# Kernel tuning notes

Hardware: AMD Instinct MI355X
Metric: run time of the kernel (lower is better)

Reference implementation:

```python
import jax, jax.numpy as jnp
import numpy as np

T, B, D, H, E = 16, 4096, 256, 512, 32
EPS = 0.1

def setup_inputs() -> dict:
    key = jax.random.key(0)
    ks = jax.random.split(key, 8)
    return {
        "term_emb": jax.random.normal(ks[0], (T, B, D), dtype=jnp.float32),
        "pred_emb": jax.random.normal(ks[1], (E, B, D), dtype=jnp.float32),
        "inv_pred_emb": jax.random.normal(ks[2], (E, B, D), dtype=jnp.float32),
        "signs": jnp.ones((E,), dtype=jnp.float32),
        "W1": jax.random.normal(ks[3], (D, H), dtype=jnp.float32) * (1.0 / np.sqrt(D)),
        "b1": jnp.zeros((H,), dtype=jnp.float32),
        "W2": jax.random.normal(ks[4], (H, D), dtype=jnp.float32) * (1.0 / np.sqrt(H)),
        "b2": jnp.zeros((D,), dtype=jnp.float32),
        "heads": jax.random.randint(ks[5], (E,), 0, T, dtype=jnp.int64),
        "tails": jax.random.randint(ks[6], (E,), 0, T, dtype=jnp.int64),
    }

def reference(term_emb, pred_emb, inv_pred_emb, signs, W1, b1, W2, b2, heads, tails):
    # gather endpoint embeddings per edge: [E, B, D]
    h = term_emb[heads]
    t = term_emb[tails]
    s = signs[:, None, None]
    # estimate_tail_emb (TransE-style NBP): translate by relation embedding
    msg_to_tail = s * (h + pred_emb)      # message along edge direction
    msg_to_head = s * (t + inv_pred_emb)  # message along inverse direction
    # scatter-add messages into per-term slots (sum aggregation)
    agg = (jax.ops.segment_sum(msg_to_tail, tails, num_segments=T)
           + jax.ops.segment_sum(msg_to_head, heads, num_segments=T))
    agg = agg + EPS * term_emb  # residual with eps
    # 1-layer MLP: Linear -> ReLU -> Linear
    hidden = jax.nn.relu(jnp.einsum('tbd,dh->tbh', agg, W1) + b1)
    out = jnp.einsum('tbh,hd->tbd', hidden, W2) + b2
    return out
```

## Files before the change

### kernel.cpp

```cpp
#include <hip/hip_runtime.h>
#include <hip/hip_bf16.h>
#include <stdint.h>

#define T_DIM 16
#define B_DIM 4096
#define D_DIM 256
#define H_DIM 512
#define E_DIM 32
#define M_DIM (T_DIM * B_DIM)
#define BD_DIM (B_DIM * D_DIM)
#define EPS_F 0.1f

#define NSLICE 16
#define SH 32
#define HS_LD 40
#define MAXS 64

typedef __attribute__((ext_vector_type(8))) short short8;
typedef __attribute__((ext_vector_type(4))) float f32x4;

#define GLOBAL_AS __attribute__((address_space(1)))
#define LDS_AS __attribute__((address_space(3)))

__device__ __forceinline__ uint32_t f2bf_rne(float x) {
  uint32_t u = __float_as_uint(x);
  return (u + 0x7fffu + ((u >> 16) & 1u)) >> 16;
}

__global__ __launch_bounds__(256) void agg_prep_kernel(
    const float* __restrict__ term, const float* __restrict__ pred,
    const float* __restrict__ inv, const float* __restrict__ signs,
    const int* __restrict__ heads, const int* __restrict__ tails,
    const float* __restrict__ W1, const float* __restrict__ W2,
    uint16_t* __restrict__ agg, uint16_t* __restrict__ W1T, uint16_t* __restrict__ W2T) {
  const int tid = threadIdx.x;
  if (blockIdx.x >= 1024) {
    const int idx = (blockIdx.x - 1024) * 256 + tid;
    const int d = idx >> 9, h = idx & (H_DIM - 1);
    W1T[h * D_DIM + d] = (uint16_t)f2bf_rne(W1[idx]);
    const int h2 = idx >> 8, d2 = idx & (D_DIM - 1);
    W2T[d2 * H_DIM + h2] = (uint16_t)f2bf_rne(W2[idx]);
    return;
  }

  __shared__ float Cm[T_DIM][T_DIM];
  __shared__ float Lsgn[T_DIM][MAXS];
  __shared__ uint64_t Lptr[T_DIM][MAXS];
  __shared__ int Lcnt[T_DIM];

  Cm[tid >> 4][tid & 15] = ((tid >> 4) == (tid & 15)) ? EPS_F : 0.f;
  if (tid < T_DIM) Lcnt[tid] = 0;
  __syncthreads();
  if (tid < E_DIM) {
    const int e = tid;
    const int hh = heads[e] & (T_DIM - 1);
    const int tt = tails[e] & (T_DIM - 1);
    const float s = signs[e];
    atomicAdd(&Cm[tt][hh], s);
    int i = atomicAdd(&Lcnt[tt], 1);
    Lsgn[tt][i] = s; Lptr[tt][i] = (uint64_t)(pred + (size_t)e * BD_DIM);
    atomicAdd(&Cm[hh][tt], s);
    i = atomicAdd(&Lcnt[hh], 1);
    Lsgn[hh][i] = s; Lptr[hh][i] = (uint64_t)(inv + (size_t)e * BD_DIM);
  }
  __syncthreads();

  const int j = (blockIdx.x * 256 + tid) * 4;

  f32x4 tr[T_DIM];
#pragma unroll
  for (int s = 0; s < T_DIM; ++s)
    tr[s] = __builtin_nontemporal_load(reinterpret_cast<const f32x4*>(term + (size_t)s * BD_DIM + j));

#pragma unroll 2
  for (int t = 0; t < T_DIM; ++t) {
    f32x4 cv[4];
#pragma unroll
    for (int q = 0; q < 4; ++q) cv[q] = *reinterpret_cast<const f32x4*>(&Cm[t][q * 4]);

    float acc[4] = {0.f, 0.f, 0.f, 0.f};
#pragma unroll
    for (int s = 0; s < T_DIM; ++s) {
      const float cs = cv[s >> 2][s & 3];
#pragma unroll
      for (int k = 0; k < 4; ++k) acc[k] += cs * tr[s][k];
    }

    const int n = Lcnt[t];
#pragma unroll 2
    for (int i = 0; i < n; ++i) {
      const float sg = Lsgn[t][i];
      const float* bp = (const float*)Lptr[t][i];
      const f32x4 p = __builtin_nontemporal_load(reinterpret_cast<const f32x4*>(bp + j));
#pragma unroll
      for (int k = 0; k < 4; ++k) acc[k] += sg * p[k];
    }

    uint2 pk;
    pk.x = f2bf_rne(acc[0]) | (f2bf_rne(acc[1]) << 16);
    pk.y = f2bf_rne(acc[2]) | (f2bf_rne(acc[3]) << 16);
    *reinterpret_cast<uint2*>(agg + (size_t)t * BD_DIM + j) = pk;
  }
}

__global__ __launch_bounds__(256, 2) void mlp_fused(
    const uint16_t* __restrict__ A,
    const uint16_t* __restrict__ W1T,
    const uint16_t* __restrict__ W2T,
    const float* __restrict__ b1, const float* __restrict__ b2,
    float* __restrict__ Out) {
  __shared__ __align__(16) uint16_t As[64 * 256];
  __shared__ __align__(16) uint16_t Hs[2][64 * HS_LD];

  const int tid = threadIdx.x;
  const int w = tid >> 6;
  const int l = tid & 63;
  const int lane16 = l & 15;
  const int quad = l >> 4;
  const int m0 = blockIdx.x * 64;

  const int wm  = (w & 1) * 32;
  const int wnA = ((w >> 1) & 1) * 16;
  const int wn2 = ((w >> 1) & 1) * 128;

#pragma unroll
  for (int p = 0; p < 8; ++p) {
    const int off = p * 2048 + tid * 8;
    const int kc = off >> 11;
    const int row = (off >> 5) & 63;
    const int c = off & 31;
    const uint16_t* g = A + (size_t)(m0 + row) * D_DIM + kc * 32 + c;
    __builtin_amdgcn_global_load_lds((const GLOBAL_AS uint32_t*)g,
                                     (LDS_AS uint32_t*)(As + off), 16, 0, 0);
  }

  short8 w1f[8];
#pragma unroll
  for (int kk = 0; kk < 8; ++kk)
    w1f[kk] = *reinterpret_cast<const short8*>(
        W1T + (size_t)(wnA + lane16) * D_DIM + kk * 32 + quad * 8);

  __syncthreads();

  f32x4 oacc[2][8];
#pragma unroll
  for (int i = 0; i < 2; ++i)
#pragma unroll
    for (int j = 0; j < 8; ++j) oacc[i][j] = (f32x4){0.f, 0.f, 0.f, 0.f};

  for (int s = 0; s < NSLICE; ++s) {
    short8 w2f[8];
#pragma unroll
    for (int j = 0; j < 8; ++j)
      w2f[j] = *reinterpret_cast<const short8*>(
          W2T + (size_t)(wn2 + j * 16 + lane16) * H_DIM + s * SH + quad * 8);

    f32x4 hacc[2];
#pragma unroll
    for (int i = 0; i < 2; ++i) hacc[i] = (f32x4){0.f, 0.f, 0.f, 0.f};
#pragma unroll
    for (int kk = 0; kk < 8; ++kk) {
      short8 af[2];
#pragma unroll
      for (int i = 0; i < 2; ++i)
        af[i] = *reinterpret_cast<const short8*>(As + kk * 2048 + (wm + i * 16 + lane16) * 32 + quad * 8);
#pragma unroll
      for (int i = 0; i < 2; ++i)
        hacc[i] = __builtin_amdgcn_mfma_f32_16x16x32_bf16(af[i], w1f[kk], hacc[i], 0, 0, 0);
    }

    {
      const int hloc = wnA + lane16;
      const float bv = b1[s * SH + hloc];
      uint16_t* hsb = Hs[s & 1];
#pragma unroll
      for (int i = 0; i < 2; ++i) {
#pragma unroll
        for (int r = 0; r < 4; ++r) {
          const int row = wm + i * 16 + quad * 4 + r;
          const float x = fmaxf(hacc[i][r] + bv, 0.f);
          hsb[row * HS_LD + hloc] = (uint16_t)f2bf_rne(x);
        }
      }
    }
    __syncthreads();

    if (s < NSLICE - 1) {
#pragma unroll
      for (int kk = 0; kk < 8; ++kk)
        w1f[kk] = *reinterpret_cast<const short8*>(
            W1T + (size_t)((s + 1) * SH + wnA + lane16) * D_DIM + kk * 32 + quad * 8);
    }

    {
      const uint16_t* hsb = Hs[s & 1];
      short8 af2[2];
#pragma unroll
      for (int i = 0; i < 2; ++i)
        af2[i] = *reinterpret_cast<const short8*>(hsb + (wm + i * 16 + lane16) * HS_LD + quad * 8);
#pragma unroll
      for (int i = 0; i < 2; ++i)
#pragma unroll
        for (int j = 0; j < 8; ++j)
          oacc[i][j] = __builtin_amdgcn_mfma_f32_16x16x32_bf16(af2[i], w2f[j], oacc[i][j], 0, 0, 0);
    }
  }

#pragma unroll
  for (int j = 0; j < 8; ++j) {
    const int col = wn2 + j * 16 + lane16;
    const float bv = b2[col];
#pragma unroll
    for (int i = 0; i < 2; ++i) {
#pragma unroll
      for (int r = 0; r < 4; ++r) {
        const int row = m0 + wm + i * 16 + quad * 4 + r;
        Out[(size_t)row * D_DIM + col] = oacc[i][j][r] + bv;
      }
    }
  }
}

extern "C" void kernel_launch(void* const* d_in, const int* in_sizes, int n_in,
                              void* d_out, int out_size, void* d_ws, size_t ws_size,
                              hipStream_t stream) {
  const float* term  = (const float*)d_in[0];
  const float* pred  = (const float*)d_in[1];
  const float* inv   = (const float*)d_in[2];
  const float* signs = (const float*)d_in[3];
  const float* W1    = (const float*)d_in[4];
  const float* b1    = (const float*)d_in[5];
  const float* W2    = (const float*)d_in[6];
  const float* b2    = (const float*)d_in[7];
  const int* heads   = (const int*)d_in[8];
  const int* tails   = (const int*)d_in[9];

  char* ws = (char*)d_ws;
  uint16_t* W1T = (uint16_t*)(ws);
  uint16_t* W2T = (uint16_t*)(ws + 262144);
  uint16_t* agg = (uint16_t*)(ws + 524288);

  agg_prep_kernel<<<dim3(1536), dim3(256), 0, stream>>>(
      term, pred, inv, signs, heads, tails, W1, W2, agg, W1T, W2T);
  mlp_fused<<<dim3(M_DIM / 64), dim3(256), 0, stream>>>(
      agg, W1T, W2T, b1, b2, (float*)d_out);
}
```

Measured before the change: 448.8 us.

## Stage MLP weight slices in double-buffered LDS and hold activations in registers

In the fused MLP kernel, the activation tile now lives in registers instead of LDS. Each 32-wide slice of W1 and W2 is copied into double-buffered LDS with async global-to-LDS loads, so all four waves share one copy rather than each wave fetching weights from global memory. The loop is software-pipelined: the first-layer GEMM for the next slice runs after the second-layer GEMM of the current slice, while later slices are prefetched. In exchange, LDS use per block grows to about 74KB and register pressure rises, which may limit occupancy.

After: 389.8 us. 1.15x faster.

```diff
diff --git a/kernel.cpp b/kernel.cpp
--- a/kernel.cpp
+++ b/kernel.cpp
@@ -109,7 +109,8 @@
     const uint16_t* __restrict__ W2T,
     const float* __restrict__ b1, const float* __restrict__ b2,
     float* __restrict__ Out) {
-  __shared__ __align__(16) uint16_t As[64 * 256];
+  __shared__ __align__(16) uint16_t Wb1[2][SH * 256];
+  __shared__ __align__(16) uint16_t Wb2[2][SH * 256];
   __shared__ __align__(16) uint16_t Hs[2][64 * HS_LD];
 
   const int tid = threadIdx.x;
@@ -123,87 +124,106 @@
   const int wnA = ((w >> 1) & 1) * 16;
   const int wn2 = ((w >> 1) & 1) * 128;
 
-#pragma unroll
-  for (int p = 0; p < 8; ++p) {
-    const int off = p * 2048 + tid * 8;
-    const int kc = off >> 11;
-    const int row = (off >> 5) & 63;
-    const int c = off & 31;
-    const uint16_t* g = A + (size_t)(m0 + row) * D_DIM + kc * 32 + c;
-    __builtin_amdgcn_global_load_lds((const GLOBAL_AS uint32_t*)g,
-                                     (LDS_AS uint32_t*)(As + off), 16, 0, 0);
-  }
-
-  short8 w1f[8];
-#pragma unroll
-  for (int kk = 0; kk < 8; ++kk)
-    w1f[kk] = *reinterpret_cast<const short8*>(
-        W1T + (size_t)(wnA + lane16) * D_DIM + kk * 32 + quad * 8);
+#define STAGE_W1(sl, buf)                                                           \
+  {                                                                                 \
+    _Pragma("unroll")                                                               \
+    for (int p = 0; p < 4; ++p) {                                                   \
+      const int off = p * 2048 + tid * 8;               \
+      const int kc = off >> 10;                                                     \
+      const int hl = (off >> 5) & 31;                                               \
+      const int c = off & 31;                                                       \
+      const uint16_t* g = W1T + (size_t)((sl) * SH + hl) * D_DIM + kc * 32 + c;     \
+      __builtin_amdgcn_global_load_lds((const GLOBAL_AS uint32_t*)g,                \
+                                       (LDS_AS uint32_t*)(Wb1[buf] + off), 16, 0, 0); \
+    }                                                                               \
+  }
+#define STAGE_W2(sl, buf)                                                           \
+  {                                                                                 \
+    _Pragma("unroll")                                                               \
+    for (int p = 0; p < 4; ++p) {                                                   \
+      const int off = p * 2048 + tid * 8;                          \
+      const int d = off >> 5;                                                       \
+      const int c = off & 31;                                                       \
+      const uint16_t* g = W2T + (size_t)d * H_DIM + (sl) * SH + c;                  \
+      __builtin_amdgcn_global_load_lds((const GLOBAL_AS uint32_t*)g,                \
+                                       (LDS_AS uint32_t*)(Wb2[buf] + off), 16, 0, 0); \
+    }                                                                               \
+  }
+
+  STAGE_W1(0, 0);
+  STAGE_W1(1, 1);
+  STAGE_W2(0, 0);
+
+  short8 af[2][8];
+#pragma unroll
+  for (int i = 0; i < 2; ++i)
+#pragma unroll
+    for (int kk = 0; kk < 8; ++kk)
+      af[i][kk] = *reinterpret_cast<const short8*>(
+          A + (size_t)(m0 + wm + i * 16 + lane16) * D_DIM + kk * 32 + quad * 8);
+
+  f32x4 oacc[2][8];
+#pragma unroll
+  for (int i = 0; i < 2; ++i)
+#pragma unroll
+    for (int j = 0; j < 8; ++j) oacc[i][j] = (f32x4){0.f, 0.f, 0.f, 0.f};
 
   __syncthreads();
 
-  f32x4 oacc[2][8];
-#pragma unroll
-  for (int i = 0; i < 2; ++i)
-#pragma unroll
-    for (int j = 0; j < 8; ++j) oacc[i][j] = (f32x4){0.f, 0.f, 0.f, 0.f};
+#define PHASE_A(sl)                                                                 \
+  {                                                                                 \
+    f32x4 hacc[2];                                                                  \
+    _Pragma("unroll")                                                               \
+    for (int i = 0; i < 2; ++i) hacc[i] = (f32x4){0.f, 0.f, 0.f, 0.f};              \
+    const uint16_t* wb = Wb1[(sl) & 1];                                             \
+    _Pragma("unroll")                                                               \
+    for (int kk = 0; kk < 8; ++kk) {                                                \
+      const short8 bfr = *reinterpret_cast<const short8*>(                          \
+          wb + kk * 1024 + (wnA + lane16) * 32 + quad * 8);                         \
+      _Pragma("unroll")                                                             \
+      for (int i = 0; i < 2; ++i)                                                   \
+        hacc[i] = __builtin_amdgcn_mfma_f32_16x16x32_bf16(af[i][kk], bfr, hacc[i], 0, 0, 0); \
+    }                                                                               \
+    const int hloc = wnA + lane16;                                                  \
+    const float bv = b1[(sl) * SH + hloc];                                          \
+    uint16_t* hsb = Hs[(sl) & 1];                                                   \
+    _Pragma("unroll")                                                               \
+    for (int i = 0; i < 2; ++i) {                                                   \
+      _Pragma("unroll")                                                             \
+      for (int r = 0; r < 4; ++r) {                                                 \
+        const int row = wm + i * 16 + quad * 4 + r;                                 \
+        const float x = fmaxf(hacc[i][r] + bv, 0.f);                                \
+        hsb[row * HS_LD + hloc] = (uint16_t)f2bf_rne(x);                            \
+      }                                                                             \
+    }                                                                               \
+  }
+
+  PHASE_A(0);
 
   for (int s = 0; s < NSLICE; ++s) {
-    short8 w2f[8];
-#pragma unroll
-    for (int j = 0; j < 8; ++j)
-      w2f[j] = *reinterpret_cast<const short8*>(
-          W2T + (size_t)(wn2 + j * 16 + lane16) * H_DIM + s * SH + quad * 8);
-
-    f32x4 hacc[2];
-#pragma unroll
-    for (int i = 0; i < 2; ++i) hacc[i] = (f32x4){0.f, 0.f, 0.f, 0.f};
-#pragma unroll
-    for (int kk = 0; kk < 8; ++kk) {
-      short8 af[2];
-#pragma unroll
-      for (int i = 0; i < 2; ++i)
-        af[i] = *reinterpret_cast<const short8*>(As + kk * 2048 + (wm + i * 16 + lane16) * 32 + quad * 8);
-#pragma unroll
-      for (int i = 0; i < 2; ++i)
-        hacc[i] = __builtin_amdgcn_mfma_f32_16x16x32_bf16(af[i], w1f[kk], hacc[i], 0, 0, 0);
-    }
-
-    {
-      const int hloc = wnA + lane16;
-      const float bv = b1[s * SH + hloc];
-      uint16_t* hsb = Hs[s & 1];
-#pragma unroll
-      for (int i = 0; i < 2; ++i) {
-#pragma unroll
-        for (int r = 0; r < 4; ++r) {
-          const int row = wm + i * 16 + quad * 4 + r;
-          const float x = fmaxf(hacc[i][r] + bv, 0.f);
-          hsb[row * HS_LD + hloc] = (uint16_t)f2bf_rne(x);
-        }
-      }
-    }
     __syncthreads();
 
-    if (s < NSLICE - 1) {
-#pragma unroll
-      for (int kk = 0; kk < 8; ++kk)
-        w1f[kk] = *reinterpret_cast<const short8*>(
-            W1T + (size_t)((s + 1) * SH + wnA + lane16) * D_DIM + kk * 32 + quad * 8);
-    }
+    if (s + 2 <= NSLICE - 1) STAGE_W1(s + 2, s & 1);
+    if (s + 1 <= NSLICE - 1) STAGE_W2(s + 1, (s + 1) & 1);
 
     {
       const uint16_t* hsb = Hs[s & 1];
-      short8 af2[2];
+      const uint16_t* wb = Wb2[s & 1];
+      short8 af2[2], w2f[8];
 #pragma unroll
       for (int i = 0; i < 2; ++i)
         af2[i] = *reinterpret_cast<const short8*>(hsb + (wm + i * 16 + lane16) * HS_LD + quad * 8);
 #pragma unroll
+      for (int j = 0; j < 8; ++j)
+        w2f[j] = *reinterpret_cast<const short8*>(wb + (wn2 + j * 16 + lane16) * 32 + quad * 8);
+#pragma unroll
       for (int i = 0; i < 2; ++i)
 #pragma unroll
         for (int j = 0; j < 8; ++j)
           oacc[i][j] = __builtin_amdgcn_mfma_f32_16x16x32_bf16(af2[i], w2f[j], oacc[i][j], 0, 0, 0);
     }
+
+    if (s + 1 <= NSLICE - 1) PHASE_A(s + 1);
   }
 
 #pragma unroll
@@ -219,6 +239,9 @@
       }
     }
   }
+#undef STAGE_W1
+#undef STAGE_W2
+#undef PHASE_A
 }
 
 extern "C" void kernel_launch(void* const* d_in, const int* in_sizes, int n_in,
```

## Restructure MLP to per-wave 16-row tiles with register A, halve agg vector width

Applied to the files above, without the earlier changes.

The fused MLP kernel now gives each wave its own 16 rows. The A tile and the W2 fragments stay in registers, and each wave has a private hidden buffer in shared memory. This removes the block-wide barrier and the large shared-memory A tile, and W2 loads are prefetched one slice ahead. In exchange, every wave now loads all the W1 and W2 fragments itself, which multiplies weight traffic per block and raises register pressure. Separately, the aggregation kernel processes 2 floats per thread instead of 4 and launches twice as many blocks, aiming for more parallelism and lower register use.

New measurement: 559.7 us. 24.7% more time.

```diff
diff --git a/kernel.cpp b/kernel.cpp
--- a/kernel.cpp
+++ b/kernel.cpp
@@ -18,6 +18,7 @@
 
 typedef __attribute__((ext_vector_type(8))) short short8;
 typedef __attribute__((ext_vector_type(4))) float f32x4;
+typedef __attribute__((ext_vector_type(2))) float f32x2;
 
 #define GLOBAL_AS __attribute__((address_space(1)))
 #define LDS_AS __attribute__((address_space(3)))
@@ -34,8 +35,8 @@
     const float* __restrict__ W1, const float* __restrict__ W2,
     uint16_t* __restrict__ agg, uint16_t* __restrict__ W1T, uint16_t* __restrict__ W2T) {
   const int tid = threadIdx.x;
-  if (blockIdx.x >= 1024) {
-    const int idx = (blockIdx.x - 1024) * 256 + tid;
+  if (blockIdx.x >= 2048) {
+    const int idx = (blockIdx.x - 2048) * 256 + tid;
     const int d = idx >> 9, h = idx & (H_DIM - 1);
     W1T[h * D_DIM + d] = (uint16_t)f2bf_rne(W1[idx]);
     const int h2 = idx >> 8, d2 = idx & (D_DIM - 1);
@@ -65,41 +66,39 @@
   }
   __syncthreads();
 
-  const int j = (blockIdx.x * 256 + tid) * 4;
-
-  f32x4 tr[T_DIM];
+  const int j = (blockIdx.x * 256 + tid) * 2;
+
+  f32x2 tr[T_DIM];
 #pragma unroll
   for (int s = 0; s < T_DIM; ++s)
-    tr[s] = __builtin_nontemporal_load(reinterpret_cast<const f32x4*>(term + (size_t)s * BD_DIM + j));
-
-#pragma unroll 2
+    tr[s] = __builtin_nontemporal_load(reinterpret_cast<const f32x2*>(term + (size_t)s * BD_DIM + j));
+
+#pragma unroll 4
   for (int t = 0; t < T_DIM; ++t) {
     f32x4 cv[4];
 #pragma unroll
     for (int q = 0; q < 4; ++q) cv[q] = *reinterpret_cast<const f32x4*>(&Cm[t][q * 4]);
 
-    float acc[4] = {0.f, 0.f, 0.f, 0.f};
+    float a0 = 0.f, a1 = 0.f;
 #pragma unroll
     for (int s = 0; s < T_DIM; ++s) {
       const float cs = cv[s >> 2][s & 3];
-#pragma unroll
-      for (int k = 0; k < 4; ++k) acc[k] += cs * tr[s][k];
+      a0 += cs * tr[s][0];
+      a1 += cs * tr[s][1];
     }
 
     const int n = Lcnt[t];
-#pragma unroll 2
+#pragma unroll 4
     for (int i = 0; i < n; ++i) {
       const float sg = Lsgn[t][i];
       const float* bp = (const float*)Lptr[t][i];
-      const f32x4 p = __builtin_nontemporal_load(reinterpret_cast<const f32x4*>(bp + j));
-#pragma unroll
-      for (int k = 0; k < 4; ++k) acc[k] += sg * p[k];
-    }
-
-    uint2 pk;
-    pk.x = f2bf_rne(acc[0]) | (f2bf_rne(acc[1]) << 16);
-    pk.y = f2bf_rne(acc[2]) | (f2bf_rne(acc[3]) << 16);
-    *reinterpret_cast<uint2*>(agg + (size_t)t * BD_DIM + j) = pk;
+      const f32x2 p = __builtin_nontemporal_load(reinterpret_cast<const f32x2*>(bp + j));
+      a0 += sg * p[0];
+      a1 += sg * p[1];
+    }
+
+    *reinterpret_cast<uint32_t*>(agg + (size_t)t * BD_DIM + j) =
+        f2bf_rne(a0) | (f2bf_rne(a1) << 16);
   }
 }
 
@@ -109,8 +108,7 @@
     const uint16_t* __restrict__ W2T,
     const float* __restrict__ b1, const float* __restrict__ b2,
     float* __restrict__ Out) {
-  __shared__ __align__(16) uint16_t As[64 * 256];
-  __shared__ __align__(16) uint16_t Hs[2][64 * HS_LD];
+  __shared__ __align__(16) uint16_t Hs[4][16 * HS_LD];
 
   const int tid = threadIdx.x;
   const int w = tid >> 6;
@@ -118,105 +116,86 @@
   const int lane16 = l & 15;
   const int quad = l >> 4;
   const int m0 = blockIdx.x * 64;
-
-  const int wm  = (w & 1) * 32;
-  const int wnA = ((w >> 1) & 1) * 16;
-  const int wn2 = ((w >> 1) & 1) * 128;
-
-#pragma unroll
-  for (int p = 0; p < 8; ++p) {
-    const int off = p * 2048 + tid * 8;
-    const int kc = off >> 11;
-    const int row = (off >> 5) & 63;
-    const int c = off & 31;
-    const uint16_t* g = A + (size_t)(m0 + row) * D_DIM + kc * 32 + c;
-    __builtin_amdgcn_global_load_lds((const GLOBAL_AS uint32_t*)g,
-                                     (LDS_AS uint32_t*)(As + off), 16, 0, 0);
-  }
-
-  short8 w1f[8];
+  const int wrow = w * 16;
+  uint16_t* hsw = Hs[w];
+
+  short8 af[8];
 #pragma unroll
   for (int kk = 0; kk < 8; ++kk)
-    w1f[kk] = *reinterpret_cast<const short8*>(
-        W1T + (size_t)(wnA + lane16) * D_DIM + kk * 32 + quad * 8);
-
-  __syncthreads();
-
-  f32x4 oacc[2][8];
-#pragma unroll
-  for (int i = 0; i < 2; ++i)
-#pragma unroll
-    for (int j = 0; j < 8; ++j) oacc[i][j] = (f32x4){0.f, 0.f, 0.f, 0.f};
-
+    af[kk] = *reinterpret_cast<const short8*>(
+        A + (size_t)(m0 + wrow + lane16) * D_DIM + kk * 32 + quad * 8);
+
+  short8 w1f[2][8];
+#pragma unroll
+  for (int j = 0; j < 2; ++j)
+#pragma unroll
+    for (int kk = 0; kk < 8; ++kk)
+      w1f[j][kk] = *reinterpret_cast<const short8*>(
+          W1T + (size_t)(j * 16 + lane16) * D_DIM + kk * 32 + quad * 8);
+
+  short8 w2f[16];
+#pragma unroll
+  for (int j = 0; j < 16; ++j)
+    w2f[j] = *reinterpret_cast<const short8*>(
+        W2T + (size_t)(j * 16 + lane16) * H_DIM + quad * 8);
+
+  f32x4 oacc[16];
+#pragma unroll
+  for (int j = 0; j < 16; ++j) oacc[j] = (f32x4){0.f, 0.f, 0.f, 0.f};
+
+#pragma unroll 1
   for (int s = 0; s < NSLICE; ++s) {
-    short8 w2f[8];
-#pragma unroll
-    for (int j = 0; j < 8; ++j)
-      w2f[j] = *reinterpret_cast<const short8*>(
-          W2T + (size_t)(wn2 + j * 16 + lane16) * H_DIM + s * SH + quad * 8);
-
     f32x4 hacc[2];
 #pragma unroll
-    for (int i = 0; i < 2; ++i) hacc[i] = (f32x4){0.f, 0.f, 0.f, 0.f};
-#pragma unroll
-    for (int kk = 0; kk < 8; ++kk) {
-      short8 af[2];
-#pragma unroll
-      for (int i = 0; i < 2; ++i)
-        af[i] = *reinterpret_cast<const short8*>(As + kk * 2048 + (wm + i * 16 + lane16) * 32 + quad * 8);
-#pragma unroll
-      for (int i = 0; i < 2; ++i)
-        hacc[i] = __builtin_amdgcn_mfma_f32_16x16x32_bf16(af[i], w1f[kk], hacc[i], 0, 0, 0);
-    }
-
-    {
-      const int hloc = wnA + lane16;
+    for (int j = 0; j < 2; ++j) hacc[j] = (f32x4){0.f, 0.f, 0.f, 0.f};
+#pragma unroll
+    for (int kk = 0; kk < 8; ++kk)
+#pragma unroll
+      for (int j = 0; j < 2; ++j)
+        hacc[j] = __builtin_amdgcn_mfma_f32_16x16x32_bf16(af[kk], w1f[j][kk], hacc[j], 0, 0, 0);
+
+#pragma unroll
+    for (int j = 0; j < 2; ++j) {
+      const int hloc = j * 16 + lane16;
       const float bv = b1[s * SH + hloc];
-      uint16_t* hsb = Hs[s & 1];
-#pragma unroll
-      for (int i = 0; i < 2; ++i) {
-#pragma unroll
-        for (int r = 0; r < 4; ++r) {
-          const int row = wm + i * 16 + quad * 4 + r;
-          const float x = fmaxf(hacc[i][r] + bv, 0.f);
-          hsb[row * HS_LD + hloc] = (uint16_t)f2bf_rne(x);
-        }
+#pragma unroll
+      for (int r = 0; r < 4; ++r) {
+        const int row = quad * 4 + r;
+        const float x = fmaxf(hacc[j][r] + bv, 0.f);
+        hsw[row * HS_LD + hloc] = (uint16_t)f2bf_rne(x);
       }
     }
-    __syncthreads();
 
     if (s < NSLICE - 1) {
 #pragma unroll
-      for (int kk = 0; kk < 8; ++kk)
-        w1f[kk] = *reinterpret_cast<const short8*>(
-            W1T + (size_t)((s + 1) * SH + wnA + lane16) * D_DIM + kk * 32 + quad * 8);
-    }
-
-    {
-      const uint16_t* hsb = Hs[s & 1];
-      short8 af2[2];
-#pragma unroll
-      for (int i = 0; i < 2; ++i)
-        af2[i] = *reinterpret_cast<const short8*>(hsb + (wm + i * 16 + lane16) * HS_LD + quad * 8);
-#pragma unroll
-      for (int i = 0; i < 2; ++i)
-#pragma unroll
-        for (int j = 0; j < 8; ++j)
-          oacc[i][j] = __builtin_amdgcn_mfma_f32_16x16x32_bf16(af2[i], w2f[j], oacc[i][j], 0, 0, 0);
-    }
-  }
-
-#pragma unroll
-  for (int j = 0; j < 8; ++j) {
-    const int col = wn2 + j * 16 + lane16;
+      for (int j = 0; j < 2; ++j)
+#pragma unroll
+        for (int kk = 0; kk < 8; ++kk)
+          w1f[j][kk] = *reinterpret_cast<const short8*>(
+              W1T + (size_t)((s + 1) * SH + j * 16 + lane16) * D_DIM + kk * 32 + quad * 8);
+    }
+
+    const short8 af2 = *reinterpret_cast<const short8*>(hsw + lane16 * HS_LD + quad * 8);
+#pragma unroll
+    for (int j = 0; j < 16; ++j)
+      oacc[j] = __builtin_amdgcn_mfma_f32_16x16x32_bf16(af2, w2f[j], oacc[j], 0, 0, 0);
+
+    if (s < NSLICE - 1) {
+#pragma unroll
+      for (int j = 0; j < 16; ++j)
+        w2f[j] = *reinterpret_cast<const short8*>(
+            W2T + (size_t)(j * 16 + lane16) * H_DIM + (s + 1) * SH + quad * 8);
+    }
+  }
+
+#pragma unroll
+  for (int j = 0; j < 16; ++j) {
+    const int col = j * 16 + lane16;
     const float bv = b2[col];
 #pragma unroll
-    for (int i = 0; i < 2; ++i) {
-#pragma unroll
-      for (int r = 0; r < 4; ++r) {
-        const int row = m0 + wm + i * 16 + quad * 4 + r;
-        Out[(size_t)row * D_DIM + col] = oacc[i][j][r] + bv;
-      }
+    for (int r = 0; r < 4; ++r) {
+      const int row = m0 + wrow + quad * 4 + r;
+      Out[(size_t)row * D_DIM + col] = oacc[j][r] + bv;
     }
   }
 }
@@ -240,7 +219,7 @@
   uint16_t* W2T = (uint16_t*)(ws + 262144);
   uint16_t* agg = (uint16_t*)(ws + 524288);
 
-  agg_prep_kernel<<<dim3(1536), dim3(256), 0, stream>>>(
+  agg_prep_kernel<<<dim3(2560), dim3(256), 0, stream>>>(
       term, pred, inv, signs, heads, tails, W1, W2, agg, W1T, W2T);
   mlp_fused<<<dim3(M_DIM / 64), dim3(256), 0, stream>>>(
       agg, W1T, W2T, b1, b2, (float*)d_out);
```
